# Optimization experiments

Measured on AMD Instinct MI355X. Metric: run time of the kernel, lower is better.

The kernel has to match this reference:

```python
import jax, jax.numpy as jnp
import numpy as np
import math

B, S, D, H = 4, 2048, 512, 8
HD = D // H  # head dim = 64

def setup_inputs() -> dict:
    key = jax.random.key(0)
    ks = jax.random.split(key, 12)
    inp = {
        'queries': jax.random.normal(ks[0], (B, S, D), jnp.float32),
        'keys': jax.random.normal(ks[1], (B, S, D), jnp.float32),
        'values': jax.random.normal(ks[2], (B, S, D), jnp.float32),
        'valid_lens': jax.random.randint(ks[3], (B,), 0, 2048, jnp.int32),
        'Wq': jax.random.normal(ks[4], (D, D), jnp.float32) / math.sqrt(D),
        'bq': jnp.zeros((D,), jnp.float32),
        'Wk': jax.random.normal(ks[5], (D, D), jnp.float32) / math.sqrt(D),
        'bk': jnp.zeros((D,), jnp.float32),
        'Wv': jax.random.normal(ks[6], (D, D), jnp.float32) / math.sqrt(D),
        'bv': jnp.zeros((D,), jnp.float32),
        'Wo': jax.random.normal(ks[7], (D, D), jnp.float32) / math.sqrt(D),
        'bo': jnp.zeros((D,), jnp.float32),
    }
    return inp

def reference(queries, keys, values, valid_lens, Wq, bq, Wk, bk, Wv, bv, Wo, bo):
    # project and split heads: [B,S,D] -> [B,H,S,HD]
    def split_heads(x):
        return x.reshape(B, S, H, HD).transpose(0, 2, 1, 3)
    q = split_heads(queries @ Wq + bq)
    k = split_heads(keys @ Wk + bk)
    v = split_heads(values @ Wv + bv)
    # scores [B,H,Sq,Sk]
    scores = jnp.einsum('bhqd,bhkd->bhqk', q, k) / math.sqrt(HD)
    # masked softmax: mask key positions >= valid_len with -1e6 (d2l semantics)
    mask = jnp.arange(S)[None, None, None, :] < valid_lens[:, None, None, None]
    scores = jnp.where(mask, scores, -1e6)
    attn = jax.nn.softmax(scores, axis=-1)
    out = jnp.einsum('bhqk,bhkd->bhqd', attn, v)  # [B,H,S,HD]
    out = out.transpose(0, 2, 1, 3).reshape(B, S, D)
    return out @ Wo + bo
```

## Files before the change

### kernel.cpp

```cpp
#include <hip/hip_runtime.h>
#include <hip/hip_bf16.h>

typedef _Float16 half8 __attribute__((ext_vector_type(8)));
typedef _Float16 half4 __attribute__((ext_vector_type(4)));
typedef float floatx4 __attribute__((ext_vector_type(4)));

#define LOG2E 1.44269504088896340736f

__device__ __forceinline__ half8 cvt8r(floatx4 a, floatx4 b) {
    half8 h;
    h[0] = (_Float16)a[0]; h[1] = (_Float16)a[1]; h[2] = (_Float16)a[2]; h[3] = (_Float16)a[3];
    h[4] = (_Float16)b[0]; h[5] = (_Float16)b[1]; h[6] = (_Float16)b[2]; h[7] = (_Float16)b[3];
    return h;
}

__global__ __launch_bounds__(256) void transpose_w_kernel(
        const float* __restrict__ Wq, const float* __restrict__ Wk,
        const float* __restrict__ Wv, const float* __restrict__ Wo,
        _Float16* __restrict__ out) {
    const float* W = (blockIdx.z == 0) ? Wq : (blockIdx.z == 1) ? Wk : (blockIdx.z == 2) ? Wv : Wo;
    _Float16* o = out + (size_t)blockIdx.z * 512 * 512;
    __shared__ __align__(16) _Float16 t[64][72];
    int r0 = blockIdx.x * 64, c0 = blockIdx.y * 64;
    int tid = threadIdx.x;
    for (int i = 0; i < 2; i++) {
        int f = i * 256 + tid;
        int row = f >> 3, seg = f & 7;
        const float* p = W + (size_t)(r0 + row) * 512 + c0 + seg * 8;
        *(half8*)&t[row][seg * 8] = cvt8r(*(const floatx4*)p, *(const floatx4*)(p + 4));
    }
    __syncthreads();
    for (int i = 0; i < 2; i++) {
        int f = i * 256 + tid;
        int crow = f >> 3, seg = f & 7;
        half8 hv;
        for (int j = 0; j < 8; j++) hv[j] = t[seg * 8 + j][crow];
        *(half8*)(o + (size_t)(c0 + crow) * 512 + r0 + seg * 8) = hv;
    }
}

__global__ __launch_bounds__(256) void gemm_qkv_kernel(
        const float* __restrict__ Xq, const float* __restrict__ Xk, const float* __restrict__ Xv,
        const _Float16* __restrict__ WTall,
        const float* __restrict__ bq, const float* __restrict__ bk, const float* __restrict__ bv,
        _Float16* __restrict__ qo, _Float16* __restrict__ ko2, _Float16* __restrict__ vto) {
    int z = blockIdx.z;
    const float* X = (z == 0) ? Xq : (z == 1) ? Xk : Xv;
    const _Float16* BT = WTall + (size_t)z * 512 * 512;
    const float* bias = (z == 0) ? bq : (z == 1) ? bk : bv;

    __shared__ __align__(16) _Float16 Asm[64][72];
    __shared__ __align__(16) _Float16 Bsm[128][72];

    int tid = threadIdx.x;
    int wave = tid >> 6, lane = tid & 63;
    int lrow = lane & 15, quad = lane >> 4;
    int mBase = blockIdx.x * 64, nBase = blockIdx.y * 128;
    int mrow = wave * 16 + lrow;

    const floatx4 fz = {0.f, 0.f, 0.f, 0.f};
    floatx4 acc[8];
    for (int i = 0; i < 8; i++) acc[i] = fz;

    int arow[2], aseg[2], brow[4], bseg[4];
    for (int i = 0; i < 2; i++) { int f = i * 256 + tid; arow[i] = f >> 3; aseg[i] = f & 7; }
    for (int i = 0; i < 4; i++) { int f = i * 256 + tid; brow[i] = f >> 3; bseg[i] = f & 7; }

    floatx4 areg[2][2];
    half8 breg[4];
    for (int i = 0; i < 2; i++) {
        const float* pa = X + (size_t)(mBase + arow[i]) * 512 + aseg[i] * 8;
        areg[i][0] = *(const floatx4*)pa;
        areg[i][1] = *(const floatx4*)(pa + 4);
    }
    for (int i = 0; i < 4; i++)
        breg[i] = *(const half8*)(BT + (size_t)(nBase + brow[i]) * 512 + bseg[i] * 8);

    for (int kb = 0; kb < 512; kb += 64) {
        for (int i = 0; i < 2; i++) *(half8*)&Asm[arow[i]][aseg[i] * 8] = cvt8r(areg[i][0], areg[i][1]);
        for (int i = 0; i < 4; i++) *(half8*)&Bsm[brow[i]][bseg[i] * 8] = breg[i];
        __syncthreads();
        if (kb + 64 < 512) {
            int kn = kb + 64;
            for (int i = 0; i < 2; i++) {
                const float* pa = X + (size_t)(mBase + arow[i]) * 512 + kn + aseg[i] * 8;
                areg[i][0] = *(const floatx4*)pa;
                areg[i][1] = *(const floatx4*)(pa + 4);
            }
            for (int i = 0; i < 4; i++)
                breg[i] = *(const half8*)(BT + (size_t)(nBase + brow[i]) * 512 + kn + bseg[i] * 8);
        }
        for (int kc = 0; kc < 2; kc++) {
            int ko_ = kc * 32 + quad * 8;
            half8 a = *(const half8*)&Asm[mrow][ko_];
            for (int nt = 0; nt < 8; nt++) {
                half8 b = *(const half8*)&Bsm[nt * 16 + lrow][ko_];
                acc[nt] = __builtin_amdgcn_mfma_f32_16x16x32_f16(a, b, acc[nt], 0, 0, 0);
            }
        }
        __syncthreads();
    }

    if (z == 2) {
        for (int nt = 0; nt < 8; nt++) {
            int gc = nBase + nt * 16 + lrow;
            float bb = bias[gc];
            int h = gc >> 6, hd = gc & 63;
            int gr = mBase + wave * 16 + quad * 4;
            int b_ = gr >> 11, s = gr & 2047;
            half4 hv;
            for (int r = 0; r < 4; r++) hv[r] = (_Float16)(acc[nt][r] + bb);
            *(half4*)(vto + (((size_t)(b_ * 8 + h) * 64 + hd) * 2048 + s)) = hv;
        }
    } else {
        _Float16* out = (z == 0) ? qo : ko2;
        for (int nt = 0; nt < 8; nt++) {
            int gc = nBase + nt * 16 + lrow;
            float bb = bias[gc];
            int h = gc >> 6, hd = gc & 63;
            for (int r = 0; r < 4; r++) {
                int gr = mBase + wave * 16 + quad * 4 + r;
                int b_ = gr >> 11, s = gr & 2047;
                out[(((size_t)b_ * 8 + h) * 2048 + s) * 64 + hd] = (_Float16)(acc[nt][r] + bb);
            }
        }
    }
}

__global__ __launch_bounds__(128) void attn_kernel(
        const _Float16* __restrict__ qws, const _Float16* __restrict__ kws, const _Float16* __restrict__ vtws,
        const int* __restrict__ vlens, _Float16* __restrict__ aout) {
    int idx = blockIdx.x;
    int b = ((idx & 3) + (idx >> 8)) & 3;
    int h = (idx >> 2) & 7;
    int q0 = ((idx >> 5) & 31) * 64;
    int bh = b * 8 + h;
    int L = vlens[b];
    bool uni = (L == 0);
    int nkt = uni ? 32 : ((L + 63) >> 6);
    int nfull = uni ? 0 : (L >> 6);
    int tid = threadIdx.x;
    int w = tid >> 6, lane = tid & 63;
    int lrow = lane & 15, quad = lane >> 4;

    __shared__ __align__(16) _Float16 ksm[64][72];
    __shared__ __align__(16) _Float16 vtsm[80][72];

    for (int i = tid; i < 15 * 36; i += 128) {
        int r = i / 36, c = i % 36;
        ((float*)&vtsm[65 + r][0])[c] = 0.0f;
    }
    if (tid < 64) vtsm[64][tid] = (_Float16)1.0f;

    const _Float16* qbase = qws + ((size_t)bh * 2048 + q0) * 64;
    const _Float16* kbase = kws + (size_t)bh * 2048 * 64;
    const _Float16* vtbase = vtws + (size_t)bh * 64 * 2048;

    half8 qf[2][2];
    for (int qt = 0; qt < 2; qt++)
        for (int kc = 0; kc < 2; kc++) {
            qf[qt][kc] = *(const half8*)(qbase + (w * 32 + qt * 16 + lrow) * 64 + kc * 32 + quad * 8);
            qf[qt][kc] = qf[qt][kc] * (_Float16)(0.125f * LOG2E);
        }

    const floatx4 fz = {0.f, 0.f, 0.f, 0.f};
    floatx4 oacc[2][5];
    for (int qt = 0; qt < 2; qt++) for (int nt = 0; nt < 5; nt++) oacc[qt][nt] = fz;

    int srow[4], sseg[4];
    for (int i = 0; i < 4; i++) { int f = i * 128 + tid; srow[i] = f >> 3; sseg[i] = f & 7; }
    half8 kreg[4], vreg[4];
    for (int i = 0; i < 4; i++) {
        kreg[i] = *(const half8*)(kbase + (i * 128 + tid) * 8);
        vreg[i] = *(const half8*)(vtbase + (size_t)srow[i] * 2048 + sseg[i] * 8);
    }

    for (int kt = 0; kt < nkt; kt++) {
        for (int i = 0; i < 4; i++) {
            *(half8*)&ksm[srow[i]][sseg[i] * 8]  = kreg[i];
            *(half8*)&vtsm[srow[i]][sseg[i] * 8] = vreg[i];
        }
        __syncthreads();
        if (kt + 1 < nkt) {
            const _Float16* ktn = kbase + (size_t)(kt + 1) * 64 * 64;
            const _Float16* vtn = vtbase + (kt + 1) * 64;
            for (int i = 0; i < 4; i++) {
                kreg[i] = *(const half8*)(ktn + (i * 128 + tid) * 8);
                vreg[i] = *(const half8*)(vtn + (size_t)srow[i] * 2048 + sseg[i] * 8);
            }
        }

        floatx4 sacc[2][4];
        for (int qt = 0; qt < 2; qt++) for (int km = 0; km < 4; km++) sacc[qt][km] = fz;
        for (int kc = 0; kc < 2; kc++) {
            int ko_ = kc * 32 + quad * 8;
            for (int km = 0; km < 4; km++) {
                half8 kf = *(const half8*)&ksm[km * 16 + lrow][ko_];
                sacc[0][km] = __builtin_amdgcn_mfma_f32_16x16x32_f16(kf, qf[0][kc], sacc[0][km], 0, 0, 0);
                sacc[1][km] = __builtin_amdgcn_mfma_f32_16x16x32_f16(kf, qf[1][kc], sacc[1][km], 0, 0, 0);
            }
        }

        half4 pf[2][4];
        if (kt < nfull) {
            for (int qt = 0; qt < 2; qt++)
                for (int km = 0; km < 4; km++)
                    for (int r = 0; r < 4; r++)
                        pf[qt][km][r] = (_Float16)exp2f(sacc[qt][km][r]);
        } else {
            int kb0 = kt * 64 + quad * 4;
            for (int km = 0; km < 4; km++) {
                int kb = kb0 + km * 16;
                for (int qt = 0; qt < 2; qt++)
                    for (int r = 0; r < 4; r++) {
                        float p = uni ? 1.0f : ((kb + r < L) ? exp2f(sacc[qt][km][r]) : 0.0f);
                        pf[qt][km][r] = (_Float16)p;
                    }
            }
        }

        for (int km = 0; km < 4; km++) {
            int kk = km * 16 + quad * 4;
            for (int nt = 0; nt < 5; nt++) {
                half4 bvf = *(const half4*)&vtsm[nt * 16 + lrow][kk];
                oacc[0][nt] = __builtin_amdgcn_mfma_f32_16x16x16f16(pf[0][km], bvf, oacc[0][nt], 0, 0, 0);
                oacc[1][nt] = __builtin_amdgcn_mfma_f32_16x16x16f16(pf[1][km], bvf, oacc[1][nt], 0, 0, 0);
            }
        }
        __syncthreads();
    }

    for (int qt = 0; qt < 2; qt++) {
        float inv[4];
        for (int r = 0; r < 4; r++)
            inv[r] = 1.0f / __shfl(oacc[qt][4][r], quad << 4, 64);
        for (int nt = 0; nt < 4; nt++) {
            for (int r = 0; r < 4; r++) {
                int s = q0 + w * 32 + qt * 16 + quad * 4 + r;
                aout[((size_t)b * 2048 + s) * 512 + h * 64 + nt * 16 + lrow] =
                    (_Float16)(oacc[qt][nt][r] * inv[r]);
            }
        }
    }
}

__global__ __launch_bounds__(256) void gemm_out_kernel(
        const _Float16* __restrict__ A, const _Float16* __restrict__ BT,
        const float* __restrict__ bias, float* __restrict__ out) {
    __shared__ __align__(16) _Float16 Asm[64][72];
    __shared__ __align__(16) _Float16 Bsm[128][72];

    int tid = threadIdx.x;
    int wave = tid >> 6, lane = tid & 63;
    int lrow = lane & 15, quad = lane >> 4;
    int mBase = blockIdx.x * 64, nBase = blockIdx.y * 128;
    int mrow = wave * 16 + lrow;

    const floatx4 fz = {0.f, 0.f, 0.f, 0.f};
    floatx4 acc[8];
    for (int i = 0; i < 8; i++) acc[i] = fz;

    int arow[2], aseg[2], brow[4], bseg[4];
    for (int i = 0; i < 2; i++) { int f = i * 256 + tid; arow[i] = f >> 3; aseg[i] = f & 7; }
    for (int i = 0; i < 4; i++) { int f = i * 256 + tid; brow[i] = f >> 3; bseg[i] = f & 7; }

    half8 areg[2], breg[4];
    for (int i = 0; i < 2; i++)
        areg[i] = *(const half8*)(A + (size_t)(mBase + arow[i]) * 512 + aseg[i] * 8);
    for (int i = 0; i < 4; i++)
        breg[i] = *(const half8*)(BT + (size_t)(nBase + brow[i]) * 512 + bseg[i] * 8);

    for (int kb = 0; kb < 512; kb += 64) {
        for (int i = 0; i < 2; i++) *(half8*)&Asm[arow[i]][aseg[i] * 8] = areg[i];
        for (int i = 0; i < 4; i++) *(half8*)&Bsm[brow[i]][bseg[i] * 8] = breg[i];
        __syncthreads();
        if (kb + 64 < 512) {
            int kn = kb + 64;
            for (int i = 0; i < 2; i++)
                areg[i] = *(const half8*)(A + (size_t)(mBase + arow[i]) * 512 + kn + aseg[i] * 8);
            for (int i = 0; i < 4; i++)
                breg[i] = *(const half8*)(BT + (size_t)(nBase + brow[i]) * 512 + kn + bseg[i] * 8);
        }
        for (int kc = 0; kc < 2; kc++) {
            int ko_ = kc * 32 + quad * 8;
            half8 a = *(const half8*)&Asm[mrow][ko_];
            for (int nt = 0; nt < 8; nt++) {
                half8 b = *(const half8*)&Bsm[nt * 16 + lrow][ko_];
                acc[nt] = __builtin_amdgcn_mfma_f32_16x16x32_f16(a, b, acc[nt], 0, 0, 0);
            }
        }
        __syncthreads();
    }

    for (int nt = 0; nt < 8; nt++) {
        int gc = nBase + nt * 16 + lrow;
        float bb = bias[gc];
        for (int r = 0; r < 4; r++) {
            int gr = mBase + wave * 16 + quad * 4 + r;
            out[(size_t)gr * 512 + gc] = acc[nt][r] + bb;
        }
    }
}

extern "C" void kernel_launch(void* const* d_in, const int* in_sizes, int n_in,
                              void* d_out, int out_size, void* d_ws, size_t ws_size,
                              hipStream_t stream) {
    const float* Q  = (const float*)d_in[0];
    const float* K  = (const float*)d_in[1];
    const float* V  = (const float*)d_in[2];
    const int*   VL = (const int*)d_in[3];
    const float* Wq = (const float*)d_in[4];
    const float* bq = (const float*)d_in[5];
    const float* Wk = (const float*)d_in[6];
    const float* bk = (const float*)d_in[7];
    const float* Wv = (const float*)d_in[8];
    const float* bv = (const float*)d_in[9];
    const float* Wo = (const float*)d_in[10];
    const float* bo = (const float*)d_in[11];

    char* ws = (char*)d_ws;
    _Float16* WT   = (_Float16*)ws;
    _Float16* qws  = (_Float16*)(ws + (size_t)(2)  * 1024 * 1024);
    _Float16* kws  = (_Float16*)(ws + (size_t)(10) * 1024 * 1024);
    _Float16* aout = (_Float16*)(ws + (size_t)(18) * 1024 * 1024);
    _Float16* vtws = (_Float16*)(ws + (size_t)(26) * 1024 * 1024);

    transpose_w_kernel<<<dim3(8, 8, 4), 256, 0, stream>>>(Wq, Wk, Wv, Wo, WT);
    gemm_qkv_kernel<<<dim3(128, 4, 3), 256, 0, stream>>>(Q, K, V, WT, bq, bk, bv, qws, kws, vtws);
    attn_kernel<<<dim3(1024, 1, 1), 128, 0, stream>>>(qws, kws, vtws, VL, aout);
    gemm_out_kernel<<<dim3(128, 4, 1), 256, 0, stream>>>(aout, WT + (size_t)3 * 512 * 512, bo, (float*)d_out);
}
```

Before: 194.1 us.

## Split attention KV range across two wave halves and skip masked K/V projections

The attention kernel now runs 256 threads per block. The two 128-thread halves each process half of the key tiles with their own shared-memory buffers, and their partial numerators and row sums are combined through shared memory before the output is normalized. Separately, the QKV projection kernel returns early for K and V row tiles that lie entirely beyond the valid length, since those keys are masked and never read. The split adds parallelism per query tile at the cost of more shared memory and a reduction step. The early exit relies on the attention kernel never reading past nkt tiles, with the L==0 case for V kept because that path reads every tile.

```diff
diff --git a/kernel.cpp b/kernel.cpp
--- a/kernel.cpp
+++ b/kernel.cpp
@@ -43,8 +43,17 @@
         const float* __restrict__ Xq, const float* __restrict__ Xk, const float* __restrict__ Xv,
         const _Float16* __restrict__ WTall,
         const float* __restrict__ bq, const float* __restrict__ bk, const float* __restrict__ bv,
+        const int* __restrict__ vlens,
         _Float16* __restrict__ qo, _Float16* __restrict__ ko2, _Float16* __restrict__ vto) {
     int z = blockIdx.z;
+    int mBase = blockIdx.x * 64, nBase = blockIdx.y * 128;
+
+    if (z >= 1) {
+        int b_ = mBase >> 11, s0 = mBase & 2047;
+        int L = vlens[b_];
+        if (s0 >= L && !(z == 2 && L == 0)) return;
+    }
+
     const float* X = (z == 0) ? Xq : (z == 1) ? Xk : Xv;
     const _Float16* BT = WTall + (size_t)z * 512 * 512;
     const float* bias = (z == 0) ? bq : (z == 1) ? bk : bv;
@@ -55,7 +64,6 @@
     int tid = threadIdx.x;
     int wave = tid >> 6, lane = tid & 63;
     int lrow = lane & 15, quad = lane >> 4;
-    int mBase = blockIdx.x * 64, nBase = blockIdx.y * 128;
     int mrow = wave * 16 + lrow;
 
     const floatx4 fz = {0.f, 0.f, 0.f, 0.f};
@@ -127,7 +135,7 @@
     }
 }
 
-__global__ __launch_bounds__(128) void attn_kernel(
+__global__ __launch_bounds__(256) void attn_kernel(
         const _Float16* __restrict__ qws, const _Float16* __restrict__ kws, const _Float16* __restrict__ vtws,
         const int* __restrict__ vlens, _Float16* __restrict__ aout) {
     int idx = blockIdx.x;
@@ -139,18 +147,28 @@
     bool uni = (L == 0);
     int nkt = uni ? 32 : ((L + 63) >> 6);
     int nfull = uni ? 0 : (L >> 6);
+    int nh = (nkt + 1) >> 1;
+
     int tid = threadIdx.x;
     int w = tid >> 6, lane = tid & 63;
     int lrow = lane & 15, quad = lane >> 4;
-
-    __shared__ __align__(16) _Float16 ksm[64][72];
-    __shared__ __align__(16) _Float16 vtsm[80][72];
-
-    for (int i = tid; i < 15 * 36; i += 128) {
+    int half = w >> 1, wq = w & 1;
+    int t128 = tid & 127;
+
+    int my_start = half * nh;
+    int my_count = half ? (nkt - nh) : nh;
+
+    __shared__ __align__(16) char smem[2 * 20736];
+    char* hbase = smem + half * 20736;
+    _Float16 (*ksm)[72]  = (_Float16(*)[72])hbase;
+    _Float16 (*vtsm)[72] = (_Float16(*)[72])(hbase + 64 * 72 * 2);
+    float (*comb)[66] = (float(*)[66])(smem + 20736);
+
+    for (int i = t128; i < 15 * 36; i += 128) {
         int r = i / 36, c = i % 36;
         ((float*)&vtsm[65 + r][0])[c] = 0.0f;
     }
-    if (tid < 64) vtsm[64][tid] = (_Float16)1.0f;
+    if (t128 < 64) vtsm[64][t128] = (_Float16)1.0f;
 
     const _Float16* qbase = qws + ((size_t)bh * 2048 + q0) * 64;
     const _Float16* kbase = kws + (size_t)bh * 2048 * 64;
@@ -159,7 +177,7 @@
     half8 qf[2][2];
     for (int qt = 0; qt < 2; qt++)
         for (int kc = 0; kc < 2; kc++) {
-            qf[qt][kc] = *(const half8*)(qbase + (w * 32 + qt * 16 + lrow) * 64 + kc * 32 + quad * 8);
+            qf[qt][kc] = *(const half8*)(qbase + (wq * 32 + qt * 16 + lrow) * 64 + kc * 32 + quad * 8);
             qf[qt][kc] = qf[qt][kc] * (_Float16)(0.125f * LOG2E);
         }
 
@@ -168,77 +186,100 @@
     for (int qt = 0; qt < 2; qt++) for (int nt = 0; nt < 5; nt++) oacc[qt][nt] = fz;
 
     int srow[4], sseg[4];
-    for (int i = 0; i < 4; i++) { int f = i * 128 + tid; srow[i] = f >> 3; sseg[i] = f & 7; }
+    for (int i = 0; i < 4; i++) { int f = i * 128 + t128; srow[i] = f >> 3; sseg[i] = f & 7; }
     half8 kreg[4], vreg[4];
-    for (int i = 0; i < 4; i++) {
-        kreg[i] = *(const half8*)(kbase + (i * 128 + tid) * 8);
-        vreg[i] = *(const half8*)(vtbase + (size_t)srow[i] * 2048 + sseg[i] * 8);
-    }
-
-    for (int kt = 0; kt < nkt; kt++) {
+    if (my_count > 0) {
+        const _Float16* kt0 = kbase + (size_t)my_start * 4096;
+        const _Float16* vt0 = vtbase + my_start * 64;
         for (int i = 0; i < 4; i++) {
-            *(half8*)&ksm[srow[i]][sseg[i] * 8]  = kreg[i];
-            *(half8*)&vtsm[srow[i]][sseg[i] * 8] = vreg[i];
-        }
-        __syncthreads();
-        if (kt + 1 < nkt) {
-            const _Float16* ktn = kbase + (size_t)(kt + 1) * 64 * 64;
+            kreg[i] = *(const half8*)(kt0 + (i * 128 + t128) * 8);
+            vreg[i] = *(const half8*)(vt0 + (size_t)srow[i] * 2048 + sseg[i] * 8);
+        }
+    }
+
+    for (int step = 0; step < nh; step++) {
+        bool active = step < my_count;
+        int kt = my_start + step;
+        if (active) {
+            for (int i = 0; i < 4; i++) {
+                *(half8*)&ksm[srow[i]][sseg[i] * 8]  = kreg[i];
+                *(half8*)&vtsm[srow[i]][sseg[i] * 8] = vreg[i];
+            }
+        }
+        __syncthreads();
+        if (active && step + 1 < my_count) {
+            const _Float16* ktn = kbase + (size_t)(kt + 1) * 4096;
             const _Float16* vtn = vtbase + (kt + 1) * 64;
             for (int i = 0; i < 4; i++) {
-                kreg[i] = *(const half8*)(ktn + (i * 128 + tid) * 8);
+                kreg[i] = *(const half8*)(ktn + (i * 128 + t128) * 8);
                 vreg[i] = *(const half8*)(vtn + (size_t)srow[i] * 2048 + sseg[i] * 8);
             }
         }
-
-        floatx4 sacc[2][4];
-        for (int qt = 0; qt < 2; qt++) for (int km = 0; km < 4; km++) sacc[qt][km] = fz;
-        for (int kc = 0; kc < 2; kc++) {
-            int ko_ = kc * 32 + quad * 8;
+        if (active) {
+            floatx4 sacc[2][4];
+            for (int qt = 0; qt < 2; qt++) for (int km = 0; km < 4; km++) sacc[qt][km] = fz;
+            for (int kc = 0; kc < 2; kc++) {
+                int ko_ = kc * 32 + quad * 8;
+                for (int km = 0; km < 4; km++) {
+                    half8 kf = *(const half8*)&ksm[km * 16 + lrow][ko_];
+                    sacc[0][km] = __builtin_amdgcn_mfma_f32_16x16x32_f16(kf, qf[0][kc], sacc[0][km], 0, 0, 0);
+                    sacc[1][km] = __builtin_amdgcn_mfma_f32_16x16x32_f16(kf, qf[1][kc], sacc[1][km], 0, 0, 0);
+                }
+            }
+
+            half4 pf[2][4];
+            if (kt < nfull) {
+                for (int qt = 0; qt < 2; qt++)
+                    for (int km = 0; km < 4; km++)
+                        for (int r = 0; r < 4; r++)
+                            pf[qt][km][r] = (_Float16)exp2f(sacc[qt][km][r]);
+            } else {
+                int kb0 = kt * 64 + quad * 4;
+                for (int km = 0; km < 4; km++) {
+                    int kb = kb0 + km * 16;
+                    for (int qt = 0; qt < 2; qt++)
+                        for (int r = 0; r < 4; r++) {
+                            float p = uni ? 1.0f : ((kb + r < L) ? exp2f(sacc[qt][km][r]) : 0.0f);
+                            pf[qt][km][r] = (_Float16)p;
+                        }
+                }
+            }
+
             for (int km = 0; km < 4; km++) {
-                half8 kf = *(const half8*)&ksm[km * 16 + lrow][ko_];
-                sacc[0][km] = __builtin_amdgcn_mfma_f32_16x16x32_f16(kf, qf[0][kc], sacc[0][km], 0, 0, 0);
-                sacc[1][km] = __builtin_amdgcn_mfma_f32_16x16x32_f16(kf, qf[1][kc], sacc[1][km], 0, 0, 0);
-            }
-        }
-
-        half4 pf[2][4];
-        if (kt < nfull) {
-            for (int qt = 0; qt < 2; qt++)
-                for (int km = 0; km < 4; km++)
-                    for (int r = 0; r < 4; r++)
-                        pf[qt][km][r] = (_Float16)exp2f(sacc[qt][km][r]);
-        } else {
-            int kb0 = kt * 64 + quad * 4;
-            for (int km = 0; km < 4; km++) {
-                int kb = kb0 + km * 16;
-                for (int qt = 0; qt < 2; qt++)
-                    for (int r = 0; r < 4; r++) {
-                        float p = uni ? 1.0f : ((kb + r < L) ? exp2f(sacc[qt][km][r]) : 0.0f);
-                        pf[qt][km][r] = (_Float16)p;
-                    }
-            }
-        }
-
-        for (int km = 0; km < 4; km++) {
-            int kk = km * 16 + quad * 4;
-            for (int nt = 0; nt < 5; nt++) {
-                half4 bvf = *(const half4*)&vtsm[nt * 16 + lrow][kk];
-                oacc[0][nt] = __builtin_amdgcn_mfma_f32_16x16x16f16(pf[0][km], bvf, oacc[0][nt], 0, 0, 0);
-                oacc[1][nt] = __builtin_amdgcn_mfma_f32_16x16x16f16(pf[1][km], bvf, oacc[1][nt], 0, 0, 0);
-            }
-        }
-        __syncthreads();
-    }
-
-    for (int qt = 0; qt < 2; qt++) {
-        float inv[4];
-        for (int r = 0; r < 4; r++)
-            inv[r] = 1.0f / __shfl(oacc[qt][4][r], quad << 4, 64);
-        for (int nt = 0; nt < 4; nt++) {
+                int kk = km * 16 + quad * 4;
+                for (int nt = 0; nt < 5; nt++) {
+                    half4 bvf = *(const half4*)&vtsm[nt * 16 + lrow][kk];
+                    oacc[0][nt] = __builtin_amdgcn_mfma_f32_16x16x16f16(pf[0][km], bvf, oacc[0][nt], 0, 0, 0);
+                    oacc[1][nt] = __builtin_amdgcn_mfma_f32_16x16x16f16(pf[1][km], bvf, oacc[1][nt], 0, 0, 0);
+                }
+            }
+        }
+        __syncthreads();
+    }
+
+    if (half == 1) {
+        for (int qt = 0; qt < 2; qt++) {
             for (int r = 0; r < 4; r++) {
-                int s = q0 + w * 32 + qt * 16 + quad * 4 + r;
-                aout[((size_t)b * 2048 + s) * 512 + h * 64 + nt * 16 + lrow] =
-                    (_Float16)(oacc[qt][nt][r] * inv[r]);
+                int row = wq * 32 + qt * 16 + quad * 4 + r;
+                for (int nt = 0; nt < 4; nt++)
+                    comb[row][nt * 16 + lrow] = oacc[qt][nt][r];
+                if (lrow == 0)
+                    comb[row][64] = oacc[qt][4][r];
+            }
+        }
+    }
+    __syncthreads();
+    if (half == 0) {
+        for (int qt = 0; qt < 2; qt++) {
+            for (int r = 0; r < 4; r++) {
+                int row = wq * 32 + qt * 16 + quad * 4 + r;
+                float sumA = __shfl(oacc[qt][4][r], quad << 4, 64);
+                float inv = 1.0f / (sumA + comb[row][64]);
+                int s = q0 + row;
+                for (int nt = 0; nt < 4; nt++) {
+                    float val = (oacc[qt][nt][r] + comb[row][nt * 16 + lrow]) * inv;
+                    aout[((size_t)b * 2048 + s) * 512 + h * 64 + nt * 16 + lrow] = (_Float16)val;
+                }
             }
         }
     }
@@ -326,7 +367,7 @@
     _Float16* vtws = (_Float16*)(ws + (size_t)(26) * 1024 * 1024);
 
     transpose_w_kernel<<<dim3(8, 8, 4), 256, 0, stream>>>(Wq, Wk, Wv, Wo, WT);
-    gemm_qkv_kernel<<<dim3(128, 4, 3), 256, 0, stream>>>(Q, K, V, WT, bq, bk, bv, qws, kws, vtws);
-    attn_kernel<<<dim3(1024, 1, 1), 128, 0, stream>>>(qws, kws, vtws, VL, aout);
+    gemm_qkv_kernel<<<dim3(128, 4, 3), 256, 0, stream>>>(Q, K, V, WT, bq, bk, bv, VL, qws, kws, vtws);
+    attn_kernel<<<dim3(1024, 1, 1), 256, 0, stream>>>(qws, kws, vtws, VL, aout);
     gemm_out_kernel<<<dim3(128, 4, 1), 256, 0, stream>>>(aout, WT + (size_t)3 * 512 * 512, bo, (float*)d_out);
 }
```

After: 194.9 us. No clear change (+0.4%).

## Skip masked K/V projection tiles and load attention fragments directly from global

Applied to the files above, without the earlier changes.

The QKV projection now exits early for K and V row tiles whose sequence positions lie at or past the batch's valid length, since the attention kernel never reads them (V is kept in full when the length is zero). The attention kernel drops its shared-memory staging and barriers. Each wave loads K and V^T MFMA fragments straight from global memory, and the row-sum column comes from an in-register ones fragment. Blocks grow to 256 threads covering 128 queries, which halves the grid. This trades LDS traffic and synchronisation for more redundant global/L2 reads across waves and no explicit prefetch overlap.

```diff
diff --git a/kernel.cpp b/kernel.cpp
--- a/kernel.cpp
+++ b/kernel.cpp
@@ -43,8 +43,17 @@
         const float* __restrict__ Xq, const float* __restrict__ Xk, const float* __restrict__ Xv,
         const _Float16* __restrict__ WTall,
         const float* __restrict__ bq, const float* __restrict__ bk, const float* __restrict__ bv,
+        const int* __restrict__ vlens,
         _Float16* __restrict__ qo, _Float16* __restrict__ ko2, _Float16* __restrict__ vto) {
     int z = blockIdx.z;
+    int mBase = blockIdx.x * 64, nBase = blockIdx.y * 128;
+
+    if (z >= 1) {
+        int b_ = mBase >> 11, s0 = mBase & 2047;
+        int L = vlens[b_];
+        if (s0 >= L && !(z == 2 && L == 0)) return;
+    }
+
     const float* X = (z == 0) ? Xq : (z == 1) ? Xk : Xv;
     const _Float16* BT = WTall + (size_t)z * 512 * 512;
     const float* bias = (z == 0) ? bq : (z == 1) ? bk : bv;
@@ -55,7 +64,6 @@
     int tid = threadIdx.x;
     int wave = tid >> 6, lane = tid & 63;
     int lrow = lane & 15, quad = lane >> 4;
-    int mBase = blockIdx.x * 64, nBase = blockIdx.y * 128;
     int mrow = wave * 16 + lrow;
 
     const floatx4 fz = {0.f, 0.f, 0.f, 0.f};
@@ -127,30 +135,22 @@
     }
 }
 
-__global__ __launch_bounds__(128) void attn_kernel(
+__global__ __launch_bounds__(256) void attn_kernel(
         const _Float16* __restrict__ qws, const _Float16* __restrict__ kws, const _Float16* __restrict__ vtws,
         const int* __restrict__ vlens, _Float16* __restrict__ aout) {
     int idx = blockIdx.x;
-    int b = ((idx & 3) + (idx >> 8)) & 3;
+    int b = ((idx & 3) + (idx >> 7)) & 3;
     int h = (idx >> 2) & 7;
-    int q0 = ((idx >> 5) & 31) * 64;
+    int q0 = ((idx >> 5) & 15) * 128;
     int bh = b * 8 + h;
     int L = vlens[b];
     bool uni = (L == 0);
     int nkt = uni ? 32 : ((L + 63) >> 6);
     int nfull = uni ? 0 : (L >> 6);
+
     int tid = threadIdx.x;
     int w = tid >> 6, lane = tid & 63;
     int lrow = lane & 15, quad = lane >> 4;
-
-    __shared__ __align__(16) _Float16 ksm[64][72];
-    __shared__ __align__(16) _Float16 vtsm[80][72];
-
-    for (int i = tid; i < 15 * 36; i += 128) {
-        int r = i / 36, c = i % 36;
-        ((float*)&vtsm[65 + r][0])[c] = 0.0f;
-    }
-    if (tid < 64) vtsm[64][tid] = (_Float16)1.0f;
 
     const _Float16* qbase = qws + ((size_t)bh * 2048 + q0) * 64;
     const _Float16* kbase = kws + (size_t)bh * 2048 * 64;
@@ -163,43 +163,36 @@
             qf[qt][kc] = qf[qt][kc] * (_Float16)(0.125f * LOG2E);
         }
 
+    half4 onesf;
+    {
+        _Float16 o1 = (lrow == 0) ? (_Float16)1.0f : (_Float16)0.0f;
+        onesf[0] = o1; onesf[1] = o1; onesf[2] = o1; onesf[3] = o1;
+    }
+
     const floatx4 fz = {0.f, 0.f, 0.f, 0.f};
     floatx4 oacc[2][5];
     for (int qt = 0; qt < 2; qt++) for (int nt = 0; nt < 5; nt++) oacc[qt][nt] = fz;
 
-    int srow[4], sseg[4];
-    for (int i = 0; i < 4; i++) { int f = i * 128 + tid; srow[i] = f >> 3; sseg[i] = f & 7; }
-    half8 kreg[4], vreg[4];
-    for (int i = 0; i < 4; i++) {
-        kreg[i] = *(const half8*)(kbase + (i * 128 + tid) * 8);
-        vreg[i] = *(const half8*)(vtbase + (size_t)srow[i] * 2048 + sseg[i] * 8);
-    }
-
     for (int kt = 0; kt < nkt; kt++) {
-        for (int i = 0; i < 4; i++) {
-            *(half8*)&ksm[srow[i]][sseg[i] * 8]  = kreg[i];
-            *(half8*)&vtsm[srow[i]][sseg[i] * 8] = vreg[i];
-        }
-        __syncthreads();
-        if (kt + 1 < nkt) {
-            const _Float16* ktn = kbase + (size_t)(kt + 1) * 64 * 64;
-            const _Float16* vtn = vtbase + (kt + 1) * 64;
-            for (int i = 0; i < 4; i++) {
-                kreg[i] = *(const half8*)(ktn + (i * 128 + tid) * 8);
-                vreg[i] = *(const half8*)(vtn + (size_t)srow[i] * 2048 + sseg[i] * 8);
-            }
-        }
+        const _Float16* ktile = kbase + (size_t)kt * 4096;
+        const _Float16* vttile = vtbase + kt * 64;
+
+        half8 kf[2][4];
+        for (int kc = 0; kc < 2; kc++)
+            for (int km = 0; km < 4; km++)
+                kf[kc][km] = *(const half8*)(ktile + (km * 16 + lrow) * 64 + kc * 32 + quad * 8);
+        half4 bvf[4][4];
+        for (int km = 0; km < 4; km++)
+            for (int nt = 0; nt < 4; nt++)
+                bvf[km][nt] = *(const half4*)(vttile + (size_t)(nt * 16 + lrow) * 2048 + km * 16 + quad * 4);
 
         floatx4 sacc[2][4];
         for (int qt = 0; qt < 2; qt++) for (int km = 0; km < 4; km++) sacc[qt][km] = fz;
-        for (int kc = 0; kc < 2; kc++) {
-            int ko_ = kc * 32 + quad * 8;
+        for (int kc = 0; kc < 2; kc++)
             for (int km = 0; km < 4; km++) {
-                half8 kf = *(const half8*)&ksm[km * 16 + lrow][ko_];
-                sacc[0][km] = __builtin_amdgcn_mfma_f32_16x16x32_f16(kf, qf[0][kc], sacc[0][km], 0, 0, 0);
-                sacc[1][km] = __builtin_amdgcn_mfma_f32_16x16x32_f16(kf, qf[1][kc], sacc[1][km], 0, 0, 0);
-            }
-        }
+                sacc[0][km] = __builtin_amdgcn_mfma_f32_16x16x32_f16(kf[kc][km], qf[0][kc], sacc[0][km], 0, 0, 0);
+                sacc[1][km] = __builtin_amdgcn_mfma_f32_16x16x32_f16(kf[kc][km], qf[1][kc], sacc[1][km], 0, 0, 0);
+            }
 
         half4 pf[2][4];
         if (kt < nfull) {
@@ -220,14 +213,13 @@
         }
 
         for (int km = 0; km < 4; km++) {
-            int kk = km * 16 + quad * 4;
-            for (int nt = 0; nt < 5; nt++) {
-                half4 bvf = *(const half4*)&vtsm[nt * 16 + lrow][kk];
-                oacc[0][nt] = __builtin_amdgcn_mfma_f32_16x16x16f16(pf[0][km], bvf, oacc[0][nt], 0, 0, 0);
-                oacc[1][nt] = __builtin_amdgcn_mfma_f32_16x16x16f16(pf[1][km], bvf, oacc[1][nt], 0, 0, 0);
-            }
-        }
-        __syncthreads();
+            for (int nt = 0; nt < 4; nt++) {
+                oacc[0][nt] = __builtin_amdgcn_mfma_f32_16x16x16f16(pf[0][km], bvf[km][nt], oacc[0][nt], 0, 0, 0);
+                oacc[1][nt] = __builtin_amdgcn_mfma_f32_16x16x16f16(pf[1][km], bvf[km][nt], oacc[1][nt], 0, 0, 0);
+            }
+            oacc[0][4] = __builtin_amdgcn_mfma_f32_16x16x16f16(pf[0][km], onesf, oacc[0][4], 0, 0, 0);
+            oacc[1][4] = __builtin_amdgcn_mfma_f32_16x16x16f16(pf[1][km], onesf, oacc[1][4], 0, 0, 0);
+        }
     }
 
     for (int qt = 0; qt < 2; qt++) {
@@ -326,7 +318,7 @@
     _Float16* vtws = (_Float16*)(ws + (size_t)(26) * 1024 * 1024);
 
     transpose_w_kernel<<<dim3(8, 8, 4), 256, 0, stream>>>(Wq, Wk, Wv, Wo, WT);
-    gemm_qkv_kernel<<<dim3(128, 4, 3), 256, 0, stream>>>(Q, K, V, WT, bq, bk, bv, qws, kws, vtws);
-    attn_kernel<<<dim3(1024, 1, 1), 128, 0, stream>>>(qws, kws, vtws, VL, aout);
+    gemm_qkv_kernel<<<dim3(128, 4, 3), 256, 0, stream>>>(Q, K, V, WT, bq, bk, bv, VL, qws, kws, vtws);
+    attn_kernel<<<dim3(512, 1, 1), 256, 0, stream>>>(qws, kws, vtws, VL, aout);
     gemm_out_kernel<<<dim3(128, 4, 1), 256, 0, stream>>>(aout, WT + (size_t)3 * 512 * 512, bo, (float*)d_out);
 }
```

After: 266.3 us. 1.37x slower.

## Skip K/V projection for masked rows and halve attention query tile

Applied to the files above, without the earlier changes.

The QKV projection kernel now returns early for K and V row tiles that lie entirely beyond the batch's valid length, since attention never reads them (V is still computed when L is zero, where attention is uniform). The attention kernel moves from 64 to 32 queries per block, giving each wave one 16-row query tile, and doubles the grid to 2048 blocks for better occupancy and load balance. The row-sum column that used to live in shared memory as a row of ones is now produced by a register-held ones fragment fed to an extra MFMA. Smaller query tiles mean each K/V tile is loaded into shared memory twice as often in total.

```diff
diff --git a/kernel.cpp b/kernel.cpp
--- a/kernel.cpp
+++ b/kernel.cpp
@@ -43,8 +43,17 @@
         const float* __restrict__ Xq, const float* __restrict__ Xk, const float* __restrict__ Xv,
         const _Float16* __restrict__ WTall,
         const float* __restrict__ bq, const float* __restrict__ bk, const float* __restrict__ bv,
+        const int* __restrict__ vlens,
         _Float16* __restrict__ qo, _Float16* __restrict__ ko2, _Float16* __restrict__ vto) {
     int z = blockIdx.z;
+    int mBase = blockIdx.x * 64, nBase = blockIdx.y * 128;
+
+    if (z >= 1) {
+        int b_ = mBase >> 11, s0 = mBase & 2047;
+        int L = vlens[b_];
+        if (s0 >= L && !(z == 2 && L == 0)) return;
+    }
+
     const float* X = (z == 0) ? Xq : (z == 1) ? Xk : Xv;
     const _Float16* BT = WTall + (size_t)z * 512 * 512;
     const float* bias = (z == 0) ? bq : (z == 1) ? bk : bv;
@@ -55,7 +64,6 @@
     int tid = threadIdx.x;
     int wave = tid >> 6, lane = tid & 63;
     int lrow = lane & 15, quad = lane >> 4;
-    int mBase = blockIdx.x * 64, nBase = blockIdx.y * 128;
     int mrow = wave * 16 + lrow;
 
     const floatx4 fz = {0.f, 0.f, 0.f, 0.f};
@@ -133,39 +141,39 @@
     int idx = blockIdx.x;
     int b = ((idx & 3) + (idx >> 8)) & 3;
     int h = (idx >> 2) & 7;
-    int q0 = ((idx >> 5) & 31) * 64;
+    int q0 = ((idx >> 5) & 63) * 32;
     int bh = b * 8 + h;
     int L = vlens[b];
     bool uni = (L == 0);
     int nkt = uni ? 32 : ((L + 63) >> 6);
     int nfull = uni ? 0 : (L >> 6);
+
     int tid = threadIdx.x;
     int w = tid >> 6, lane = tid & 63;
     int lrow = lane & 15, quad = lane >> 4;
 
     __shared__ __align__(16) _Float16 ksm[64][72];
-    __shared__ __align__(16) _Float16 vtsm[80][72];
-
-    for (int i = tid; i < 15 * 36; i += 128) {
-        int r = i / 36, c = i % 36;
-        ((float*)&vtsm[65 + r][0])[c] = 0.0f;
-    }
-    if (tid < 64) vtsm[64][tid] = (_Float16)1.0f;
+    __shared__ __align__(16) _Float16 vtsm[64][72];
 
     const _Float16* qbase = qws + ((size_t)bh * 2048 + q0) * 64;
     const _Float16* kbase = kws + (size_t)bh * 2048 * 64;
     const _Float16* vtbase = vtws + (size_t)bh * 64 * 2048;
 
-    half8 qf[2][2];
-    for (int qt = 0; qt < 2; qt++)
-        for (int kc = 0; kc < 2; kc++) {
-            qf[qt][kc] = *(const half8*)(qbase + (w * 32 + qt * 16 + lrow) * 64 + kc * 32 + quad * 8);
-            qf[qt][kc] = qf[qt][kc] * (_Float16)(0.125f * LOG2E);
-        }
+    half8 qf[2];
+    for (int kc = 0; kc < 2; kc++) {
+        qf[kc] = *(const half8*)(qbase + (w * 16 + lrow) * 64 + kc * 32 + quad * 8);
+        qf[kc] = qf[kc] * (_Float16)(0.125f * LOG2E);
+    }
+
+    half4 onesf;
+    {
+        _Float16 o1 = (lrow == 0) ? (_Float16)1.0f : (_Float16)0.0f;
+        onesf[0] = o1; onesf[1] = o1; onesf[2] = o1; onesf[3] = o1;
+    }
 
     const floatx4 fz = {0.f, 0.f, 0.f, 0.f};
-    floatx4 oacc[2][5];
-    for (int qt = 0; qt < 2; qt++) for (int nt = 0; nt < 5; nt++) oacc[qt][nt] = fz;
+    floatx4 oacc[5];
+    for (int nt = 0; nt < 5; nt++) oacc[nt] = fz;
 
     int srow[4], sseg[4];
     for (int i = 0; i < 4; i++) { int f = i * 128 + tid; srow[i] = f >> 3; sseg[i] = f & 7; }
@@ -182,7 +190,7 @@
         }
         __syncthreads();
         if (kt + 1 < nkt) {
-            const _Float16* ktn = kbase + (size_t)(kt + 1) * 64 * 64;
+            const _Float16* ktn = kbase + (size_t)(kt + 1) * 4096;
             const _Float16* vtn = vtbase + (kt + 1) * 64;
             for (int i = 0; i < 4; i++) {
                 kreg[i] = *(const half8*)(ktn + (i * 128 + tid) * 8);
@@ -190,56 +198,52 @@
             }
         }
 
-        floatx4 sacc[2][4];
-        for (int qt = 0; qt < 2; qt++) for (int km = 0; km < 4; km++) sacc[qt][km] = fz;
+        floatx4 sacc[4];
+        for (int km = 0; km < 4; km++) sacc[km] = fz;
         for (int kc = 0; kc < 2; kc++) {
             int ko_ = kc * 32 + quad * 8;
             for (int km = 0; km < 4; km++) {
                 half8 kf = *(const half8*)&ksm[km * 16 + lrow][ko_];
-                sacc[0][km] = __builtin_amdgcn_mfma_f32_16x16x32_f16(kf, qf[0][kc], sacc[0][km], 0, 0, 0);
-                sacc[1][km] = __builtin_amdgcn_mfma_f32_16x16x32_f16(kf, qf[1][kc], sacc[1][km], 0, 0, 0);
-            }
-        }
-
-        half4 pf[2][4];
+                sacc[km] = __builtin_amdgcn_mfma_f32_16x16x32_f16(kf, qf[kc], sacc[km], 0, 0, 0);
+            }
+        }
+
+        half4 pf[4];
         if (kt < nfull) {
-            for (int qt = 0; qt < 2; qt++)
-                for (int km = 0; km < 4; km++)
-                    for (int r = 0; r < 4; r++)
-                        pf[qt][km][r] = (_Float16)exp2f(sacc[qt][km][r]);
+            for (int km = 0; km < 4; km++)
+                for (int r = 0; r < 4; r++)
+                    pf[km][r] = (_Float16)exp2f(sacc[km][r]);
         } else {
             int kb0 = kt * 64 + quad * 4;
             for (int km = 0; km < 4; km++) {
                 int kb = kb0 + km * 16;
-                for (int qt = 0; qt < 2; qt++)
-                    for (int r = 0; r < 4; r++) {
-                        float p = uni ? 1.0f : ((kb + r < L) ? exp2f(sacc[qt][km][r]) : 0.0f);
-                        pf[qt][km][r] = (_Float16)p;
-                    }
+                for (int r = 0; r < 4; r++) {
+                    float p = uni ? 1.0f : ((kb + r < L) ? exp2f(sacc[km][r]) : 0.0f);
+                    pf[km][r] = (_Float16)p;
+                }
             }
         }
 
         for (int km = 0; km < 4; km++) {
             int kk = km * 16 + quad * 4;
-            for (int nt = 0; nt < 5; nt++) {
+            for (int nt = 0; nt < 4; nt++) {
                 half4 bvf = *(const half4*)&vtsm[nt * 16 + lrow][kk];
-                oacc[0][nt] = __builtin_amdgcn_mfma_f32_16x16x16f16(pf[0][km], bvf, oacc[0][nt], 0, 0, 0);
-                oacc[1][nt] = __builtin_amdgcn_mfma_f32_16x16x16f16(pf[1][km], bvf, oacc[1][nt], 0, 0, 0);
-            }
-        }
-        __syncthreads();
-    }
-
-    for (int qt = 0; qt < 2; qt++) {
-        float inv[4];
-        for (int r = 0; r < 4; r++)
-            inv[r] = 1.0f / __shfl(oacc[qt][4][r], quad << 4, 64);
-        for (int nt = 0; nt < 4; nt++) {
-            for (int r = 0; r < 4; r++) {
-                int s = q0 + w * 32 + qt * 16 + quad * 4 + r;
-                aout[((size_t)b * 2048 + s) * 512 + h * 64 + nt * 16 + lrow] =
-                    (_Float16)(oacc[qt][nt][r] * inv[r]);
-            }
+                oacc[nt] = __builtin_amdgcn_mfma_f32_16x16x16f16(pf[km], bvf, oacc[nt], 0, 0, 0);
+            }
+            oacc[4] = __builtin_amdgcn_mfma_f32_16x16x16f16(pf[km], onesf, oacc[4], 0, 0, 0);
+        }
+        __syncthreads();
+    }
+
+    float inv[4];
+    for (int r = 0; r < 4; r++)
+        inv[r] = 1.0f / __shfl(oacc[4][r], quad << 4, 64);
+
+    for (int nt = 0; nt < 4; nt++) {
+        for (int r = 0; r < 4; r++) {
+            int s = q0 + w * 16 + quad * 4 + r;
+            aout[((size_t)b * 2048 + s) * 512 + h * 64 + nt * 16 + lrow] =
+                (_Float16)(oacc[nt][r] * inv[r]);
         }
     }
 }
@@ -326,7 +330,7 @@
     _Float16* vtws = (_Float16*)(ws + (size_t)(26) * 1024 * 1024);
 
     transpose_w_kernel<<<dim3(8, 8, 4), 256, 0, stream>>>(Wq, Wk, Wv, Wo, WT);
-    gemm_qkv_kernel<<<dim3(128, 4, 3), 256, 0, stream>>>(Q, K, V, WT, bq, bk, bv, qws, kws, vtws);
-    attn_kernel<<<dim3(1024, 1, 1), 128, 0, stream>>>(qws, kws, vtws, VL, aout);
+    gemm_qkv_kernel<<<dim3(128, 4, 3), 256, 0, stream>>>(Q, K, V, WT, bq, bk, bv, VL, qws, kws, vtws);
+    attn_kernel<<<dim3(2048, 1, 1), 128, 0, stream>>>(qws, kws, vtws, VL, aout);
     gemm_out_kernel<<<dim3(128, 4, 1), 256, 0, stream>>>(aout, WT + (size_t)3 * 512 * 512, bo, (float*)d_out);
 }
```

After: 191.1 us. Within noise of the previous version (-1.5%).
